# Performance work log

Measured on AMD Instinct MI355X. Metric: run time of the kernel, lower is better.

Reference implementation:

```python
import jax, jax.numpy as jnp
import numpy as np

DICE_W = 0.7
BOUNDARY_W = 0.3
SMOOTH = 1.0
# Sobel x and y stacked as a 2-output-channel conv kernel, shape (O=2, I=1, 3, 3)
SOBEL = jnp.array([
    [[[-1.0, 0.0, 1.0], [-2.0, 0.0, 2.0], [-1.0, 0.0, 1.0]]],
    [[[-1.0, -2.0, -1.0], [0.0, 0.0, 0.0], [1.0, 2.0, 1.0]]],
], dtype=jnp.float32)


def _boundary(x):
    # x: [B, C, H, W] -> binary boundary map via Sobel magnitude > 0.5
    B, C, H, W = x.shape
    xf = x.reshape(B * C, 1, H, W)  # fold channels into batch: one batched conv
    g = jax.lax.conv_general_dilated(
        xf, SOBEL, window_strides=(1, 1), padding='SAME',
        dimension_numbers=('NCHW', 'OIHW', 'NCHW'))  # [B*C, 2, H, W]
    mag = jnp.sqrt(g[:, 0] ** 2 + g[:, 1] ** 2)
    return (mag > 0.5).astype(x.dtype).reshape(B, C, H, W)


def _bce_mean(p, t):
    # torch F.binary_cross_entropy clamps log terms at -100 (here p,t in {0,1})
    log_p = jnp.maximum(jnp.log(p), -100.0)
    log_1mp = jnp.maximum(jnp.log(1.0 - p), -100.0)
    return jnp.mean(-(t * log_p + (1.0 - t) * log_1mp))


def setup_inputs() -> dict:
    key = jax.random.key(0)
    k1, k2 = jax.random.split(key)
    B, C, H, W = 8, 4, 512, 512
    logits = jax.random.normal(k1, (B, C, H, W), dtype=jnp.float32)
    targets = jnp.round(jax.random.uniform(k2, (B, C, H, W), dtype=jnp.float32))
    class_weights = jnp.array([1.0, 2.0, 1.5, 0.5], dtype=jnp.float32)
    return {"logits": logits, "targets": targets, "class_weights": class_weights}


def reference(logits, targets, class_weights):
    B, C = logits.shape[0], logits.shape[1]
    probs = jax.nn.sigmoid(logits)

    # Boundary loss
    pred_b = _boundary(probs)
    targ_b = _boundary(targets)
    boundary_loss = _bce_mean(pred_b, targ_b)

    # Class-weighted Dice loss (per-class DiceLoss, vectorized over classes)
    p = probs.reshape(B, C, -1)
    t = targets.reshape(B, C, -1)
    inter = jnp.sum(p * t, axis=-1)                              # [B, C]
    dice = (2.0 * inter + SMOOTH) / (jnp.sum(p, -1) + jnp.sum(t, -1) + SMOOTH)
    class_dice = 1.0 - jnp.mean(dice, axis=0)                    # [C]
    dice_loss = jnp.sum(class_weights * class_dice) / jnp.sum(class_weights)

    return DICE_W * dice_loss + BOUNDARY_W * boundary_loss
```

## Files before the change

### kernel.cpp

```cpp
#include <hip/hip_runtime.h>


#define H_ 512
#define W_ 512
#define NIMG 32
#define NPIXF 8388608.0f
#define R_ 4
#define NBLK 1024

__device__ __forceinline__ float sigf(float x) {
    return __builtin_amdgcn_rcpf(1.f + __expf(-x));
}

__launch_bounds__(256, 2)
__global__ void fused_loss_kernel(const float* __restrict__ logits,
                                  const float* __restrict__ targets,
                                  float4* __restrict__ part) {
    const int tid  = threadIdx.x;
    const int wid  = tid >> 6, lane = tid & 63;
    const int bx   = blockIdx.x;
    const int img  = bx >> 5;
    const int seg  = ((bx & 31) << 2) | wid;
    const int y0   = seg << 2;

    const float* Lp = logits  + (size_t)img * (H_ * W_) + (lane << 3);
    const float* Tp = targets + (size_t)img * (H_ * W_) + (lane << 3);

    float p[5][8], t[5][8];

    auto loadrow = [&](int gy, int s) {
        if ((unsigned)gy < (unsigned)H_) {
            const float4 va = *(const float4*)(Lp + gy * W_);
            const float4 vb = *(const float4*)(Lp + gy * W_ + 4);
            const float4 vc = *(const float4*)(Tp + gy * W_);
            const float4 vd = *(const float4*)(Tp + gy * W_ + 4);
            p[s][0] = sigf(va.x); p[s][1] = sigf(va.y);
            p[s][2] = sigf(va.z); p[s][3] = sigf(va.w);
            p[s][4] = sigf(vb.x); p[s][5] = sigf(vb.y);
            p[s][6] = sigf(vb.z); p[s][7] = sigf(vb.w);
            t[s][0] = vc.x; t[s][1] = vc.y; t[s][2] = vc.z; t[s][3] = vc.w;
            t[s][4] = vd.x; t[s][5] = vd.y; t[s][6] = vd.z; t[s][7] = vd.w;
        } else {
            #pragma unroll
            for (int k = 0; k < 8; ++k) { p[s][k] = 0.f; t[s][k] = 0.f; }
        }
    };

    loadrow(y0 - 1, 0);
    loadrow(y0,     1);
    loadrow(y0 + 1, 2);
    loadrow(y0 + 2, 3);

    float li = 0.f, lp = 0.f, lt = 0.f;
    int mi = 0;

    #pragma unroll
    for (int i = 0; i < R_; ++i) {
        if (i < 2) loadrow(y0 + 3 + i, (4 + i) % 5);
        const int sA = i % 5, sB = (i + 1) % 5, sC = (i + 2) % 5;

        float Tc[8], Sc[8], Tt[8], St[8];
        #pragma unroll
        for (int k = 0; k < 8; ++k) {
            Tc[k] = (p[sA][k] + p[sC][k]) + 2.f * p[sB][k];
            Sc[k] = p[sC][k] - p[sA][k];
            Tt[k] = (t[sA][k] + t[sC][k]) + 2.f * t[sB][k];
            St[k] = t[sC][k] - t[sA][k];
        }
        float TL = __shfl_up(Tc[7], 1, 64), TR = __shfl_down(Tc[0], 1, 64);
        float SL = __shfl_up(Sc[7], 1, 64), SR = __shfl_down(Sc[0], 1, 64);
        float UL = __shfl_up(Tt[7], 1, 64), UR = __shfl_down(Tt[0], 1, 64);
        float VL = __shfl_up(St[7], 1, 64), VR = __shfl_down(St[0], 1, 64);
        if (lane == 0)  { TL = 0.f; SL = 0.f; UL = 0.f; VL = 0.f; }
        if (lane == 63) { TR = 0.f; SR = 0.f; UR = 0.f; VR = 0.f; }

        #pragma unroll
        for (int k = 0; k < 8; ++k) {
            const float tl = (k == 0) ? TL : Tc[k - 1];
            const float tr = (k == 7) ? TR : Tc[k + 1];
            const float sl = (k == 0) ? SL : Sc[k - 1];
            const float sr = (k == 7) ? SR : Sc[k + 1];
            const float gx = tr - tl;
            const float gy = (sl + sr) + 2.f * Sc[k];
            const int pb = (gx * gx + gy * gy) > 0.25f;

            const float ul = (k == 0) ? UL : Tt[k - 1];
            const float ur = (k == 7) ? UR : Tt[k + 1];
            const float vl = (k == 0) ? VL : St[k - 1];
            const float vr = (k == 7) ? VR : St[k + 1];
            const float hx = ur - ul;
            const float hy = (vl + vr) + 2.f * St[k];
            const int tb = (hx * hx + hy * hy) > 0.25f;

            mi += pb ^ tb;
            const float pv = p[sB][k], tv = t[sB][k];
            lp += pv; lt += tv; li += pv * tv;
        }
    }
    float lm = (float)mi;

    #pragma unroll
    for (int off = 32; off > 0; off >>= 1) {
        li += __shfl_down(li, off, 64);
        lp += __shfl_down(lp, off, 64);
        lt += __shfl_down(lt, off, 64);
        lm += __shfl_down(lm, off, 64);
    }
    __shared__ float red[4][4];
    if (lane == 0) { red[wid][0] = li; red[wid][1] = lp; red[wid][2] = lt; red[wid][3] = lm; }
    __syncthreads();
    if (tid == 0) {
        float a = 0.f, b = 0.f, c = 0.f, d = 0.f;
        #pragma unroll
        for (int w = 0; w < 4; ++w) {
            a += red[w][0]; b += red[w][1]; c += red[w][2]; d += red[w][3];
        }
        part[bx] = make_float4(a, b, c, d);
    }
}

__global__ void finalize_kernel(const float4* __restrict__ part,
                                const float* __restrict__ cw,
                                float* __restrict__ out) {
    __shared__ float s_i[NIMG], s_p[NIMG], s_t[NIMG], s_m[NIMG];
    const int tid = threadIdx.x;
    float4 v = part[tid];
    float vi = v.x, vp = v.y, vt = v.z, vm = v.w;
    #pragma unroll
    for (int off = 16; off > 0; off >>= 1) {
        vi += __shfl_down(vi, off, 32);
        vp += __shfl_down(vp, off, 32);
        vt += __shfl_down(vt, off, 32);
        vm += __shfl_down(vm, off, 32);
    }
    if ((tid & 31) == 0) {
        const int img = tid >> 5;
        s_i[img] = vi; s_p[img] = vp; s_t[img] = vt; s_m[img] = vm;
    }
    __syncthreads();
    if (tid == 0) {
        float mm = 0.f;
        for (int i = 0; i < NIMG; ++i) mm += s_m[i];
        float wsum = 0.f, dl = 0.f;
        for (int c = 0; c < 4; ++c) {
            float md = 0.f;
            for (int b = 0; b < 8; ++b) {
                const int id = b * 4 + c;
                md += (2.f * s_i[id] + 1.f) / (s_p[id] + s_t[id] + 1.f);
            }
            md *= 0.125f;
            dl += cw[c] * (1.f - md);
            wsum += cw[c];
        }
        out[0] = 0.7f * (dl / wsum) + 0.3f * (100.f * mm / NPIXF);
    }
}

extern "C" void kernel_launch(void* const* d_in, const int* in_sizes, int n_in,
                              void* d_out, int out_size, void* d_ws, size_t ws_size,
                              hipStream_t stream) {
    const float* logits  = (const float*)d_in[0];
    const float* targets = (const float*)d_in[1];
    const float* cw      = (const float*)d_in[2];
    float* out = (float*)d_out;
    float4* part = (float4*)d_ws;

    fused_loss_kernel<<<NBLK, 256, 0, stream>>>(logits, targets, part);
    finalize_kernel<<<1, NBLK, 0, stream>>>(part, cw, out);
}
```

Measured before the change: 101.1 us.

## Bitpack binary targets and pre-shuffle halo columns per row to cut stencil work

```diff
diff --git a/kernel.cpp b/kernel.cpp
--- a/kernel.cpp
+++ b/kernel.cpp
@@ -12,7 +12,7 @@
     return __builtin_amdgcn_rcpf(1.f + __expf(-x));
 }
 
-__launch_bounds__(256, 2)
+__launch_bounds__(256, 4)
 __global__ void fused_loss_kernel(const float* __restrict__ logits,
                                   const float* __restrict__ targets,
                                   float4* __restrict__ part) {
@@ -26,7 +26,8 @@
     const float* Lp = logits  + (size_t)img * (H_ * W_) + (lane << 3);
     const float* Tp = targets + (size_t)img * (H_ * W_) + (lane << 3);
 
-    float p[5][8], t[5][8];
+    float p[5][10];
+    unsigned int win[5];
 
     auto loadrow = [&](int gy, int s) {
         if ((unsigned)gy < (unsigned)H_) {
@@ -34,15 +35,26 @@
             const float4 vb = *(const float4*)(Lp + gy * W_ + 4);
             const float4 vc = *(const float4*)(Tp + gy * W_);
             const float4 vd = *(const float4*)(Tp + gy * W_ + 4);
-            p[s][0] = sigf(va.x); p[s][1] = sigf(va.y);
-            p[s][2] = sigf(va.z); p[s][3] = sigf(va.w);
-            p[s][4] = sigf(vb.x); p[s][5] = sigf(vb.y);
-            p[s][6] = sigf(vb.z); p[s][7] = sigf(vb.w);
-            t[s][0] = vc.x; t[s][1] = vc.y; t[s][2] = vc.z; t[s][3] = vc.w;
-            t[s][4] = vd.x; t[s][5] = vd.y; t[s][6] = vd.z; t[s][7] = vd.w;
+            p[s][1] = sigf(va.x); p[s][2] = sigf(va.y);
+            p[s][3] = sigf(va.z); p[s][4] = sigf(va.w);
+            p[s][5] = sigf(vb.x); p[s][6] = sigf(vb.y);
+            p[s][7] = sigf(vb.z); p[s][8] = sigf(vb.w);
+            unsigned int m =  (vc.x > 0.5f ? 1u : 0u)       | (vc.y > 0.5f ? 2u : 0u)
+                           | (vc.z > 0.5f ? 4u : 0u)        | (vc.w > 0.5f ? 8u : 0u)
+                           | (vd.x > 0.5f ? 16u : 0u)       | (vd.y > 0.5f ? 32u : 0u)
+                           | (vd.z > 0.5f ? 64u : 0u)       | (vd.w > 0.5f ? 128u : 0u);
+            float pl = __shfl_up(p[s][8], 1, 64);
+            float pr = __shfl_down(p[s][1], 1, 64);
+            unsigned int ml = __shfl_up(m, 1, 64);
+            unsigned int mr = __shfl_down(m, 1, 64);
+            if (lane == 0)  { pl = 0.f; ml = 0u; }
+            if (lane == 63) { pr = 0.f; mr = 0u; }
+            p[s][0] = pl; p[s][9] = pr;
+            win[s] = (m << 1) | ((ml >> 7) & 1u) | ((mr & 1u) << 9);
         } else {
             #pragma unroll
-            for (int k = 0; k < 8; ++k) { p[s][k] = 0.f; t[s][k] = 0.f; }
+            for (int k = 0; k < 10; ++k) p[s][k] = 0.f;
+            win[s] = 0u;
         }
     };
 
@@ -51,52 +63,49 @@
     loadrow(y0 + 1, 2);
     loadrow(y0 + 2, 3);
 
-    float li = 0.f, lp = 0.f, lt = 0.f;
-    int mi = 0;
+    float li = 0.f, lp = 0.f;
+    int mi = 0, tcnt = 0;
 
     #pragma unroll
     for (int i = 0; i < R_; ++i) {
         if (i < 2) loadrow(y0 + 3 + i, (4 + i) % 5);
         const int sA = i % 5, sB = (i + 1) % 5, sC = (i + 2) % 5;
 
-        float Tc[8], Sc[8], Tt[8], St[8];
+        float Tc[10], Sc[10];
         #pragma unroll
-        for (int k = 0; k < 8; ++k) {
-            Tc[k] = (p[sA][k] + p[sC][k]) + 2.f * p[sB][k];
-            Sc[k] = p[sC][k] - p[sA][k];
-            Tt[k] = (t[sA][k] + t[sC][k]) + 2.f * t[sB][k];
-            St[k] = t[sC][k] - t[sA][k];
+        for (int j = 0; j < 10; ++j) {
+            Tc[j] = (p[sA][j] + p[sC][j]) + 2.f * p[sB][j];
+            Sc[j] = p[sC][j] - p[sA][j];
         }
-        float TL = __shfl_up(Tc[7], 1, 64), TR = __shfl_down(Tc[0], 1, 64);
-        float SL = __shfl_up(Sc[7], 1, 64), SR = __shfl_down(Sc[0], 1, 64);
-        float UL = __shfl_up(Tt[7], 1, 64), UR = __shfl_down(Tt[0], 1, 64);
-        float VL = __shfl_up(St[7], 1, 64), VR = __shfl_down(St[0], 1, 64);
-        if (lane == 0)  { TL = 0.f; SL = 0.f; UL = 0.f; VL = 0.f; }
-        if (lane == 63) { TR = 0.f; SR = 0.f; UR = 0.f; VR = 0.f; }
+        const unsigned int wA = win[sA], wB = win[sB], wC = win[sC];
+        int Tt[10], St[10];
+        #pragma unroll
+        for (int j = 0; j < 10; ++j) {
+            const int a = (int)((wA >> j) & 1u);
+            const int b = (int)((wB >> j) & 1u);
+            const int c = (int)((wC >> j) & 1u);
+            Tt[j] = a + 2 * b + c;
+            St[j] = c - a;
+        }
 
         #pragma unroll
         for (int k = 0; k < 8; ++k) {
-            const float tl = (k == 0) ? TL : Tc[k - 1];
-            const float tr = (k == 7) ? TR : Tc[k + 1];
-            const float sl = (k == 0) ? SL : Sc[k - 1];
-            const float sr = (k == 7) ? SR : Sc[k + 1];
-            const float gx = tr - tl;
-            const float gy = (sl + sr) + 2.f * Sc[k];
+            const float gx = Tc[k + 2] - Tc[k];
+            const float gy = (Sc[k] + Sc[k + 2]) + 2.f * Sc[k + 1];
             const int pb = (gx * gx + gy * gy) > 0.25f;
 
-            const float ul = (k == 0) ? UL : Tt[k - 1];
-            const float ur = (k == 7) ? UR : Tt[k + 1];
-            const float vl = (k == 0) ? VL : St[k - 1];
-            const float vr = (k == 7) ? VR : St[k + 1];
-            const float hx = ur - ul;
-            const float hy = (vl + vr) + 2.f * St[k];
-            const int tb = (hx * hx + hy * hy) > 0.25f;
+            const int hx = Tt[k + 2] - Tt[k];
+            const int hy = (St[k] + St[k + 2]) + 2 * St[k + 1];
+            const int tb = ((hx | hy) != 0) ? 1 : 0;
 
             mi += pb ^ tb;
-            const float pv = p[sB][k], tv = t[sB][k];
-            lp += pv; lt += tv; li += pv * tv;
+            const float pv = p[sB][k + 1];
+            lp += pv;
+            if ((wB >> (k + 1)) & 1u) li += pv;
         }
+        tcnt += __popc(wB & 0x1FEu);
     }
+    float lt = (float)tcnt;
     float lm = (float)mi;
 
     #pragma unroll
```

Result: slower. 130.6 us (+29.2%).
